# Optimization experiments

Hardware: AMD Instinct MI355X
Metric: run time of the kernel (lower is better)

## Reference

```python
import jax, jax.numpy as jnp
import numpy as np

NGRAM_N = 4

def ngram_repeat_mask(toks, n):
    # toks: [B, S] int32. Mark positions j..j+n-1 for every ngram starting at
    # j (j in range(S-n)) that already appeared at an earlier start position.
    B, S = toks.shape
    P = S - n  # number of ngram start positions, matching range(len(x)-n)
    win = jnp.arange(P)[:, None] + jnp.arange(n)[None, :]  # [P, n]
    G = toks[:, win]                                        # [B, P, n]
    eq = (G[:, :, None, :] == G[:, None, :, :]).all(-1)     # [B, P, P]
    prev = jnp.tril(jnp.ones((P, P), dtype=bool), k=-1)     # j' < j
    repeated = (eq & prev[None]).any(-1)                    # [B, P]
    # dilate forward over the ngram window: mask[j:j+n] = 1 if repeated[j]
    shifted = jnp.stack([jnp.pad(repeated, ((0, 0), (k, S - P - k)))
                         for k in range(n)], axis=0)        # [n, B, S]
    return shifted.any(0).astype(jnp.float32)               # [B, S]

def setup_inputs() -> dict:
    key = jax.random.key(0)
    B, V, S = 8, 32000, 512
    pred = jax.random.normal(key, (B, V, S), dtype=jnp.float32)
    return {"pred": pred}

def reference(pred):
    # pred: [B, V, S] logits
    B = pred.shape[0]
    pred_toks = jnp.argmax(pred, axis=1)                    # [B, S] int
    pred_lprobs_full = jax.nn.log_softmax(pred, axis=1)     # [B, V, S]
    # gather log-prob of the argmax token at each position -> [B, S]
    pred_lprobs = jnp.take_along_axis(pred_lprobs_full, pred_toks[:, None, :], axis=1)[:, 0, :]
    one_minus_probs = jnp.clip(1.0 - jnp.exp(pred_lprobs), 1e-20, None)
    mask = ngram_repeat_mask(pred_toks, NGRAM_N)            # [B, S] float
    loss = (-jnp.log(one_minus_probs) * mask).sum() / B
    return loss
```

## Files before the change

### kernel.cpp

```cpp
#include <hip/hip_runtime.h>
#include <math.h>

#define BB 8
#define VV 32000
#define SS 512
#define NCHUNK 125
#define CHUNK 256
#define NCOL (BB * SS)
#define NGRAM 4
#define PP (SS - NGRAM)
#define NREAL (BB * NCHUNK)

typedef float vfloat4 __attribute__((ext_vector_type(4)));

__global__ __launch_bounds__(256) void colstats_kernel(const float* __restrict__ pred,
                                                       float* __restrict__ pmax,
                                                       float* __restrict__ psum,
                                                       int* __restrict__ pidx) {
    const int bid = blockIdx.x;
    const int b   = bid / NCHUNK;
    const int c   = bid - b * NCHUNK;
    const int tid = threadIdx.x;
    const int vo  = tid >> 7;
    const int s   = (tid & 127) << 2;
    const int v0  = c * CHUNK;

    float m0 = -INFINITY, m1 = -INFINITY, m2 = -INFINITY, m3 = -INFINITY;
    float a0 = 0.f, a1 = 0.f, a2 = 0.f, a3 = 0.f;
    int   i0 = 0, i1 = 0, i2 = 0, i3 = 0;

    const float L2E = 1.4426950408889634f;
    const vfloat4* ptr = (const vfloat4*)(pred + ((size_t)(b * VV + v0 + vo)) * SS + s);
    int v = v0 + vo;
#pragma unroll 8
    for (int k = 0; k < CHUNK / 2; ++k) {
        const vfloat4 x = __builtin_nontemporal_load(ptr);
        ptr += (2 * SS) / 4;
        a0 += __builtin_amdgcn_exp2f(x.x * L2E);
        a1 += __builtin_amdgcn_exp2f(x.y * L2E);
        a2 += __builtin_amdgcn_exp2f(x.z * L2E);
        a3 += __builtin_amdgcn_exp2f(x.w * L2E);
        if (x.x > m0) { m0 = x.x; i0 = v; }
        if (x.y > m1) { m1 = x.y; i1 = v; }
        if (x.z > m2) { m2 = x.z; i2 = v; }
        if (x.w > m3) { m3 = x.w; i3 = v; }
        v += 2;
    }

    __shared__ float smax[256][4];
    __shared__ float ssum[256][4];
    __shared__ int   sidx[256][4];
    smax[tid][0] = m0; smax[tid][1] = m1; smax[tid][2] = m2; smax[tid][3] = m3;
    ssum[tid][0] = a0; ssum[tid][1] = a1; ssum[tid][2] = a2; ssum[tid][3] = a3;
    sidx[tid][0] = i0; sidx[tid][1] = i1; sidx[tid][2] = i2; sidx[tid][3] = i3;
    __syncthreads();

    if (tid < 128) {
        const int o = tid + 128;
        float m[4]  = {smax[tid][0], smax[tid][1], smax[tid][2], smax[tid][3]};
        float a[4]  = {ssum[tid][0], ssum[tid][1], ssum[tid][2], ssum[tid][3]};
        int   ix[4] = {sidx[tid][0], sidx[tid][1], sidx[tid][2], sidx[tid][3]};
#pragma unroll
        for (int j = 0; j < 4; ++j) {
            const float om = smax[o][j];
            const int   oi = sidx[o][j];
            a[j] += ssum[o][j];
            if (om > m[j] || (om == m[j] && oi < ix[j])) { m[j] = om; ix[j] = oi; }
        }
        const size_t ob = (size_t)c * NCOL + (size_t)b * SS + (size_t)s;
#pragma unroll
        for (int j = 0; j < 4; ++j) {
            pmax[ob + j] = m[j];
            psum[ob + j] = a[j];
            pidx[ob + j] = ix[j];
        }
    }
}

__global__ void zero_kernel(float* out) { out[0] = 0.0f; }

__global__ __launch_bounds__(512) void finalize_mask_kernel(const float* __restrict__ pmax,
                                                            const float* __restrict__ psum,
                                                            const int* __restrict__ pidx,
                                                            float* __restrict__ out) {
    const int b   = blockIdx.x;
    const int tid = threadIdx.x;
    const int col = b * SS + tid;

    float m = -INFINITY, sum = 0.f;
    int   idx = 0x7fffffff;
#pragma unroll 5
    for (int c = 0; c < NCHUNK; ++c) {
        const int off = c * NCOL + col;
        const float cm = pmax[off];
        const int   ci = pidx[off];
        sum += psum[off];
        if (cm > m || (cm == m && ci < idx)) { m = cm; idx = ci; }
    }
    const float lprob = m - logf(sum);
    const float p = expf(lprob);
    float om1 = 1.0f - p;
    if (om1 < 1e-20f) om1 = 1e-20f;

    __shared__ int   tk[SS];
    __shared__ int   rep[SS];
    __shared__ float pn[SS];
    tk[tid]  = idx;
    pn[tid]  = -logf(om1);
    rep[tid] = 0;
    __syncthreads();

    if (tid < PP) {
        const int c0 = tk[tid], c1 = tk[tid + 1], c2 = tk[tid + 2], c3 = tk[tid + 3];
        int r = 0;
        for (int j = 0; j < tid; ++j) {
            if (tk[j] == c0 && tk[j + 1] == c1 && tk[j + 2] == c2 && tk[j + 3] == c3) {
                r = 1; break;
            }
        }
        rep[tid] = r;
    }
    __syncthreads();

    float local = 0.f;
    {
        int msk = 0;
#pragma unroll
        for (int k = 0; k < NGRAM; ++k) {
            const int i = tid - k;
            if (i >= 0 && i < PP && rep[i]) msk = 1;
        }
        if (msk) local += pn[tid];
    }

    for (int off = 32; off > 0; off >>= 1) local += __shfl_down(local, off, 64);
    __shared__ float wsum[8];
    const int lane = tid & 63, wid = tid >> 6;
    if (lane == 0) wsum[wid] = local;
    __syncthreads();
    if (tid == 0) {
        float t = 0.f;
#pragma unroll
        for (int w = 0; w < 8; ++w) t += wsum[w];
        atomicAdd(out, t * (1.0f / (float)BB));
    }
}

extern "C" void kernel_launch(void* const* d_in, const int* in_sizes, int n_in,
                              void* d_out, int out_size, void* d_ws, size_t ws_size,
                              hipStream_t stream) {
    const float* pred = (const float*)d_in[0];
    float* out = (float*)d_out;
    char* ws = (char*)d_ws;

    const size_t partN = (size_t)NCHUNK * NCOL;
    float* pmax = (float*)ws;
    float* psum = (float*)(ws + partN * 4);
    int*   pidx = (int*)  (ws + partN * 8);

    colstats_kernel<<<NREAL, 256, 0, stream>>>(pred, pmax, psum, pidx);
    zero_kernel<<<1, 1, 0, stream>>>(out);
    finalize_mask_kernel<<<BB, 512, 0, stream>>>(pmax, psum, pidx, out);
}
```

Measured before the change: 719.5 us.

## Split the chunk combine into a wide kernel and hash n-grams for repeat detection

The per-column reduction over vocab chunks moves out of the 8-block finalize kernel into a new combine kernel with 128 blocks. Each block splits the chunk loop across 8 thread groups and writes the token and penalty per column. The finalize kernel packs each 4-gram into one 64-bit key, relying on the vocab fitting in 15 bits, and compares keys branchlessly instead of making four shared-memory compares with an early exit. The zero-init kernel is folded into colstats, chunking changes to 128x250 so the block index is decoded with shifts, and max and sum are stored as float2. The cost is an extra launch and an extra round trip through the workspace for the token and penalty arrays.

```diff
diff --git a/kernel.cpp b/kernel.cpp
--- a/kernel.cpp
+++ b/kernel.cpp
@@ -4,22 +4,22 @@
 #define BB 8
 #define VV 32000
 #define SS 512
-#define NCHUNK 125
-#define CHUNK 256
+#define NCHUNK 128
+#define CHUNK 250
 #define NCOL (BB * SS)
 #define NGRAM 4
 #define PP (SS - NGRAM)
-#define NREAL (BB * NCHUNK)
 
 typedef float vfloat4 __attribute__((ext_vector_type(4)));
 
 __global__ __launch_bounds__(256) void colstats_kernel(const float* __restrict__ pred,
-                                                       float* __restrict__ pmax,
-                                                       float* __restrict__ psum,
-                                                       int* __restrict__ pidx) {
+                                                       float2* __restrict__ pms,
+                                                       int* __restrict__ pidx,
+                                                       float* __restrict__ out) {
     const int bid = blockIdx.x;
-    const int b   = bid / NCHUNK;
-    const int c   = bid - b * NCHUNK;
+    if (bid == 0 && threadIdx.x == 0) out[0] = 0.0f;
+    const int b   = bid >> 7;
+    const int c   = bid & 127;
     const int tid = threadIdx.x;
     const int vo  = tid >> 7;
     const int s   = (tid & 127) << 2;
@@ -32,7 +32,7 @@
     const float L2E = 1.4426950408889634f;
     const vfloat4* ptr = (const vfloat4*)(pred + ((size_t)(b * VV + v0 + vo)) * SS + s);
     int v = v0 + vo;
-#pragma unroll 8
+#pragma unroll 5
     for (int k = 0; k < CHUNK / 2; ++k) {
         const vfloat4 x = __builtin_nontemporal_load(ptr);
         ptr += (2 * SS) / 4;
@@ -67,57 +67,92 @@
             a[j] += ssum[o][j];
             if (om > m[j] || (om == m[j] && oi < ix[j])) { m[j] = om; ix[j] = oi; }
         }
-        const size_t ob = (size_t)c * NCOL + (size_t)b * SS + (size_t)s;
+        const size_t ob = (size_t)c * NCOL + (size_t)b * SS + (size_t)(tid << 2);
 #pragma unroll
         for (int j = 0; j < 4; ++j) {
-            pmax[ob + j] = m[j];
-            psum[ob + j] = a[j];
+            float2 t; t.x = m[j]; t.y = a[j];
+            pms[ob + j]  = t;
             pidx[ob + j] = ix[j];
         }
     }
 }
 
-__global__ void zero_kernel(float* out) { out[0] = 0.0f; }
-
-__global__ __launch_bounds__(512) void finalize_mask_kernel(const float* __restrict__ pmax,
-                                                            const float* __restrict__ psum,
-                                                            const int* __restrict__ pidx,
+__global__ __launch_bounds__(256) void combine_kernel(const float2* __restrict__ pms,
+                                                      const int* __restrict__ pidx,
+                                                      int* __restrict__ tok,
+                                                      float* __restrict__ pen) {
+    const int tid = threadIdx.x;
+    const int cl  = tid & 31;
+    const int sl  = tid >> 5;
+    const int col = (blockIdx.x << 5) + cl;
+
+    float m = -INFINITY, sum = 0.f;
+    int   idx = 0x7fffffff;
+#pragma unroll 4
+    for (int c = sl * 16; c < sl * 16 + 16; ++c) {
+        const int off = c * NCOL + col;
+        const float2 ms = pms[off];
+        const int    ci = pidx[off];
+        sum += ms.y;
+        if (ms.x > m || (ms.x == m && ci < idx)) { m = ms.x; idx = ci; }
+    }
+
+    __shared__ float sm[8][32];
+    __shared__ float ss[8][32];
+    __shared__ int   si[8][32];
+    sm[sl][cl] = m; ss[sl][cl] = sum; si[sl][cl] = idx;
+    __syncthreads();
+
+    if (tid < 32) {
+        float M = sm[0][tid], S = ss[0][tid];
+        int   I = si[0][tid];
+#pragma unroll
+        for (int q = 1; q < 8; ++q) {
+            const float om = sm[q][tid];
+            const int   oi = si[q][tid];
+            S += ss[q][tid];
+            if (om > M || (om == M && oi < I)) { M = om; I = oi; }
+        }
+        const float lprob = M - logf(S);
+        const float p = expf(lprob);
+        float om1 = 1.0f - p;
+        if (om1 < 1e-20f) om1 = 1e-20f;
+        const int g = (blockIdx.x << 5) + tid;
+        tok[g] = I;
+        pen[g] = -logf(om1);
+    }
+}
+
+__global__ __launch_bounds__(512) void finalize_mask_kernel(const int* __restrict__ tok,
+                                                            const float* __restrict__ pen,
                                                             float* __restrict__ out) {
     const int b   = blockIdx.x;
     const int tid = threadIdx.x;
-    const int col = b * SS + tid;
-
-    float m = -INFINITY, sum = 0.f;
-    int   idx = 0x7fffffff;
-#pragma unroll 5
-    for (int c = 0; c < NCHUNK; ++c) {
-        const int off = c * NCOL + col;
-        const float cm = pmax[off];
-        const int   ci = pidx[off];
-        sum += psum[off];
-        if (cm > m || (cm == m && ci < idx)) { m = cm; idx = ci; }
-    }
-    const float lprob = m - logf(sum);
-    const float p = expf(lprob);
-    float om1 = 1.0f - p;
-    if (om1 < 1e-20f) om1 = 1e-20f;
-
-    __shared__ int   tk[SS];
-    __shared__ int   rep[SS];
-    __shared__ float pn[SS];
-    tk[tid]  = idx;
-    pn[tid]  = -logf(om1);
+    const int g   = b * SS + tid;
+    const int   t  = tok[g];
+    const float pv = pen[g];
+
+    __shared__ int tk[SS];
+    __shared__ unsigned long long hh[PP];
+    __shared__ int rep[SS];
+    tk[tid]  = t;
     rep[tid] = 0;
     __syncthreads();
 
     if (tid < PP) {
-        const int c0 = tk[tid], c1 = tk[tid + 1], c2 = tk[tid + 2], c3 = tk[tid + 3];
+        const unsigned long long h = (unsigned long long)tk[tid]
+            | ((unsigned long long)tk[tid + 1] << 15)
+            | ((unsigned long long)tk[tid + 2] << 30)
+            | ((unsigned long long)tk[tid + 3] << 45);
+        hh[tid] = h;
+    }
+    __syncthreads();
+
+    if (tid < PP) {
+        const unsigned long long h = hh[tid];
         int r = 0;
-        for (int j = 0; j < tid; ++j) {
-            if (tk[j] == c0 && tk[j + 1] == c1 && tk[j + 2] == c2 && tk[j + 3] == c3) {
-                r = 1; break;
-            }
-        }
+#pragma unroll 4
+        for (int j = 0; j < tid; ++j) r |= (hh[j] == h);
         rep[tid] = r;
     }
     __syncthreads();
@@ -130,7 +165,7 @@
             const int i = tid - k;
             if (i >= 0 && i < PP && rep[i]) msk = 1;
         }
-        if (msk) local += pn[tid];
+        if (msk) local = pv;
     }
 
     for (int off = 32; off > 0; off >>= 1) local += __shfl_down(local, off, 64);
@@ -139,10 +174,10 @@
     if (lane == 0) wsum[wid] = local;
     __syncthreads();
     if (tid == 0) {
-        float t = 0.f;
-#pragma unroll
-        for (int w = 0; w < 8; ++w) t += wsum[w];
-        atomicAdd(out, t * (1.0f / (float)BB));
+        float tt = 0.f;
+#pragma unroll
+        for (int w = 0; w < 8; ++w) tt += wsum[w];
+        atomicAdd(out, tt * (1.0f / (float)BB));
     }
 }
 
@@ -154,11 +189,12 @@
     char* ws = (char*)d_ws;
 
     const size_t partN = (size_t)NCHUNK * NCOL;
-    float* pmax = (float*)ws;
-    float* psum = (float*)(ws + partN * 4);
-    int*   pidx = (int*)  (ws + partN * 8);
-
-    colstats_kernel<<<NREAL, 256, 0, stream>>>(pred, pmax, psum, pidx);
-    zero_kernel<<<1, 1, 0, stream>>>(out);
-    finalize_mask_kernel<<<BB, 512, 0, stream>>>(pmax, psum, pidx, out);
-}
+    float2* pms  = (float2*)ws;
+    int*    pidx = (int*)(ws + partN * 8);
+    int*    tok  = (int*)(ws + partN * 12);
+    float*  pen  = (float*)(ws + partN * 12 + NCOL * 4);
+
+    colstats_kernel<<<BB * NCHUNK, 256, 0, stream>>>(pred, pms, pidx, out);
+    combine_kernel<<<NCOL / 32, 256, 0, stream>>>(pms, pidx, tok, pen);
+    finalize_mask_kernel<<<BB, 512, 0, stream>>>(tok, pen, out);
+}
```

After: 645.1 us. 10.3% less time.
